# Kernel tuning notes

Measured on AMD Instinct MI355X. Metric: run time of the kernel, lower is better.

## Reference

```python
import jax, jax.numpy as jnp
import numpy as np

FORE_TH = 0.5
BACK_TH = 0.4
MAX_FOR_TARGET = True
FOREGROUND_ONLY = False  # return both foreground and background masks


def _cxcywh_to_xyxy(b):
    cx, cy, w, h = b[..., 0], b[..., 1], b[..., 2], b[..., 3]
    return jnp.stack([cx - w * 0.5, cy - h * 0.5, cx + w * 0.5, cy + h * 0.5], axis=-1)


def _batch_iou(anchors_xyxy, boxes_xyxy):
    # anchors_xyxy: [A,4], boxes_xyxy: [B,T,4] -> ious [B,A,T]
    a = anchors_xyxy[None, :, None, :]   # [1,A,1,4]
    b = boxes_xyxy[:, None, :, :]        # [B,1,T,4]
    lt = jnp.maximum(a[..., :2], b[..., :2])
    rb = jnp.minimum(a[..., 2:], b[..., 2:])
    wh = jnp.clip(rb - lt, 0.0)
    inter = wh[..., 0] * wh[..., 1]                                   # [B,A,T]
    area_a = (a[..., 2] - a[..., 0]) * (a[..., 3] - a[..., 1])
    area_b = (b[..., 2] - b[..., 0]) * (b[..., 3] - b[..., 1])
    return inter / (area_a + area_b - inter + 1e-9)


def setup_inputs() -> dict:
    key = jax.random.key(0)
    k1, k2 = jax.random.split(key)
    labels = jax.random.uniform(k1, (8, 64, 84), dtype=jnp.float32)
    anchors = jax.random.uniform(k2, (1, 100000, 4), dtype=jnp.float32)
    return {"labels": labels, "anchors": anchors}


def reference(labels, anchors):
    # labels: [B, T, 4+C] (cxcywh + class), anchors: [1, A, 4] (cxcywh)
    B = labels.shape[0]
    a_xyxy = _cxcywh_to_xyxy(anchors[0])           # [A,4]
    b_xyxy = _cxcywh_to_xyxy(labels[..., :4])      # [B,T,4]
    ious = _batch_iou(a_xyxy, b_xyxy)              # [B,A,T]

    max_iou_anchor = jnp.max(ious, axis=2)         # [B,A] best IoU per anchor
    target_for_anchor = jnp.argmax(ious, axis=2)   # [B,A] best target per anchor

    fore_mask = max_iou_anchor >= FORE_TH          # [B,A]
    if MAX_FOR_TARGET:
        anchor_for_target = jnp.argmax(ious, axis=1)        # [B,T] best anchor per target
        batch_idx = jnp.arange(B)[:, None]
        fm_t = jnp.zeros(fore_mask.shape, dtype=bool).at[batch_idx, anchor_for_target].set(True)
        fore_mask = jnp.logical_or(fore_mask, fm_t)

    back_mask = jnp.logical_not(fore_mask)
    if BACK_TH is not None:
        back_mask = jnp.logical_and(back_mask, max_iou_anchor < BACK_TH)

    # label[target_for_anchor] per batch -> [B, A, 4+C]
    assigned_target = jnp.take_along_axis(labels, target_for_anchor[..., None], axis=1)

    # Fixed-shape equivalent of the original list-of-dicts with nonzero():
    # (foreground mask, background mask, per-anchor assigned labels).
    return fore_mask, back_mask, assigned_target
```

## Files before the change

### kernel.cpp

```cpp
#include <hip/hip_runtime.h>
#include <stdint.h>

typedef unsigned long long u64;

#define N_ANCH 100000
#define BATCH 8
#define NTGT 64
#define NFEAT 84
#define BLK 256
#define NWAVE (BLK / 64)
#define NBX ((N_ANCH + BLK - 1) / BLK)
#define GCHUNK (NFEAT / 4)

template <bool FULL>
__device__ __forceinline__ void iou_loop(
    const int tid, const int wave, const int n, const bool valid,
    const float4* __restrict__ tbox, const float* __restrict__ sarea,
    u64* __restrict__ board, const float* __restrict__ anchors, u64& bestA)
{
#pragma clang fp contract(off)
    const int nld = FULL ? n : (valid ? n : 0);
    const float4 ab = *(const float4*)(anchors + (size_t)nld * 4);
    const float ax1 = ab.x - ab.z * 0.5f;
    const float ay1 = ab.y - ab.w * 0.5f;
    const float ax2 = ab.x + ab.z * 0.5f;
    const float ay2 = ab.y + ab.w * 0.5f;
    const float areaA = (ax2 - ax1) * (ay2 - ay1);
    const u64 pn = (u64)(0xFFFFFFFFu - (uint32_t)n);

    for (int s = 0; s < NTGT; ++s) {
        const int t = (tid + s) & (NTGT - 1);
        const float4 tb = tbox[t];
        const float areaB = sarea[t];

        const float w = fmaxf(fminf(ax2, tb.z) - fmaxf(ax1, tb.x), 0.0f);
        const float h = fmaxf(fminf(ay2, tb.w) - fmaxf(ay1, tb.y), 0.0f);
        const float inter = w * h;
        const float iou = inter / (((areaA + areaB) - inter) + 1e-9f);
        const uint32_t ib = __float_as_uint(iou);

        const u64 pa = ((u64)ib << 32) | (u64)(63 - t);
        bestA = pa > bestA ? pa : bestA;

        u64 c = ((u64)ib << 32) | pn;
        if (!FULL) c = valid ? c : 0ull;
        atomicMax(&board[(size_t)wave * NTGT + t], c);
    }
}

__global__ __launch_bounds__(BLK) void fused_kernel(
    const float* __restrict__ labels,
    const float* __restrict__ anchors,
    float* __restrict__ out_fore,
    float* __restrict__ out_back,
    float* __restrict__ out_assigned,
    u64* __restrict__ ws_part)
{
#pragma clang fp contract(off)
    __shared__ float4 tbox[NTGT];
    __shared__ float sarea[NTGT];
    __shared__ u64 board[NWAVE * NTGT];
    __shared__ int sidx[BLK];

    const int b    = blockIdx.y;
    const int bx   = blockIdx.x;
    const int tid  = threadIdx.x;
    const int wave = tid >> 6;

    if (tid < NTGT) {
        const float4 box = *(const float4*)(labels + ((size_t)b * NTGT + tid) * NFEAT);
        const float x1 = box.x - box.z * 0.5f;
        const float y1 = box.y - box.w * 0.5f;
        const float x2 = box.x + box.z * 0.5f;
        const float y2 = box.y + box.w * 0.5f;
        tbox[tid] = make_float4(x1, y1, x2, y2);
        sarea[tid] = (x2 - x1) * (y2 - y1);
    }
    board[tid] = 0ull;
    __syncthreads();

    const int n = bx * BLK + tid;
    u64 bestA = 0ull;
    bool valid = true;
    if (bx != NBX - 1) {
        iou_loop<true>(tid, wave, n, true, tbox, sarea, board, anchors, bestA);
    } else {
        valid = (n < N_ANCH);
        iou_loop<false>(tid, wave, n, valid, tbox, sarea, board, anchors, bestA);
    }

    if (valid) {
        const float mi = __uint_as_float((uint32_t)(bestA >> 32));
        const int   bt = 63 - (int)(bestA & 0xFFFFFFFFull);
        const bool fore = (mi >= 0.5f);
        const bool back = (!fore) && (mi < 0.4f);
        const size_t o = (size_t)b * N_ANCH + n;
        out_fore[o] = fore ? 1.0f : 0.0f;
        out_back[o] = back ? 1.0f : 0.0f;
        sidx[tid] = bt;
    } else {
        sidx[tid] = 0;
    }
    __syncthreads();

    if (tid < NTGT) {
        const u64 m0 = board[tid];
        const u64 m1 = board[NTGT + tid];
        const u64 m2 = board[2 * NTGT + tid];
        const u64 m3 = board[3 * NTGT + tid];
        const u64 a = m0 > m1 ? m0 : m1;
        const u64 c = m2 > m3 ? m2 : m3;
        ws_part[((size_t)b * NTGT + tid) * NBX + bx] = a > c ? a : c;
    }

    const float* lab_b = labels + (size_t)b * NTGT * NFEAT;
    float* out_b = out_assigned + ((size_t)b * N_ANCH + (size_t)bx * BLK) * NFEAT;
    for (int i = tid; i < BLK * GCHUNK; i += BLK) {
        const int nl = i / GCHUNK;
        const int k  = i - nl * GCHUNK;
        if (bx * BLK + nl < N_ANCH) {
            const int t = sidx[nl];
            const float4 v = *(const float4*)(lab_b + (size_t)t * NFEAT + k * 4);
            *(float4*)(out_b + (size_t)nl * NFEAT + (size_t)k * 4) = v;
        }
    }
}

__global__ __launch_bounds__(64) void fixup_kernel(
    const u64* __restrict__ ws_part,
    float* __restrict__ out_fore,
    float* __restrict__ out_back)
{
    const int bt   = blockIdx.x;
    const int lane = threadIdx.x;
    const u64* p = ws_part + (size_t)bt * NBX;

    u64 best = 0ull;
    for (int i = lane; i < NBX; i += 64) {
        const u64 v = p[i];
        best = v > best ? v : best;
    }
    for (int off = 32; off > 0; off >>= 1) {
        const u64 o = __shfl_down(best, off, 64);
        best = o > best ? o : best;
    }
    if (lane == 0) {
        const uint32_t n = 0xFFFFFFFFu - (uint32_t)(best & 0xFFFFFFFFull);
        const int b = bt >> 6;
        const size_t o = (size_t)b * N_ANCH + n;
        out_fore[o] = 1.0f;
        out_back[o] = 0.0f;
    }
}

extern "C" void kernel_launch(void* const* d_in, const int* in_sizes, int n_in,
                              void* d_out, int out_size, void* d_ws, size_t ws_size,
                              hipStream_t stream) {
    const float* labels  = (const float*)d_in[0];
    const float* anchors = (const float*)d_in[1];

    float* out_fore     = (float*)d_out;
    float* out_back     = out_fore + (size_t)BATCH * N_ANCH;
    float* out_assigned = out_back + (size_t)BATCH * N_ANCH;

    u64* ws_part = (u64*)d_ws;

    dim3 gridA(NBX, BATCH);
    fused_kernel<<<gridA, BLK, 0, stream>>>(labels, anchors, out_fore, out_back,
                                            out_assigned, ws_part);

    fixup_kernel<<<BATCH * NTGT, 64, 0, stream>>>(ws_part, out_fore, out_back);
}
```

Baseline: 294.7 us.

## Process 1024 anchors per block, pair IoU atomics, overlap gather with compute

Each block now handles 1024 anchors (four per thread) instead of 256. Two anchors share each shared-memory atomicMax on the per-target board, which halves the atomic traffic. The label gather for the first half is interleaved with the IoU loop for the second half, so the stores can overlap compute. Output stores become nontemporal. Fewer blocks means fewer partial results for the fixup pass, at the cost of more registers and less parallelism per block.

```diff
diff --git a/kernel.cpp b/kernel.cpp
--- a/kernel.cpp
+++ b/kernel.cpp
@@ -2,6 +2,7 @@
 #include <stdint.h>
 
 typedef unsigned long long u64;
+typedef __attribute__((__vector_size__(16))) float vfloat4;
 
 #define N_ANCH 100000
 #define BATCH 8
@@ -9,98 +10,149 @@
 #define NFEAT 84
 #define BLK 256
 #define NWAVE (BLK / 64)
-#define NBX ((N_ANCH + BLK - 1) / BLK)
+#define APB 1024
+#define NBX ((N_ANCH + APB - 1) / APB)
 #define GCHUNK (NFEAT / 4)
+#define HALF (APB / 2)
+#define SITER (HALF * GCHUNK / BLK)
+
+struct Anch { float x1, y1, x2, y2, area; u64 pn; };
+
+__device__ __forceinline__ Anch make_anch(float4 ab, int n) {
+#pragma clang fp contract(off)
+    Anch a;
+    a.x1 = ab.x - ab.z * 0.5f;
+    a.y1 = ab.y - ab.w * 0.5f;
+    a.x2 = ab.x + ab.z * 0.5f;
+    a.y2 = ab.y + ab.w * 0.5f;
+    a.area = (a.x2 - a.x1) * (a.y2 - a.y1);
+    a.pn = (u64)(0xFFFFFFFFu - (uint32_t)n);
+    return a;
+}
+
+__device__ __forceinline__ uint32_t iou_bits(const Anch& a, float4 tb, float areaB) {
+#pragma clang fp contract(off)
+    const float w = fmaxf(fminf(a.x2, tb.z) - fmaxf(a.x1, tb.x), 0.0f);
+    const float h = fmaxf(fminf(a.y2, tb.w) - fmaxf(a.y1, tb.y), 0.0f);
+    const float inter = w * h;
+    const float iou = inter / (((a.area + areaB) - inter) + 1e-9f);
+    return __float_as_uint(iou);
+}
 
 template <bool FULL>
-__device__ __forceinline__ void iou_loop(
-    const int tid, const int wave, const int n, const bool valid,
+__device__ __forceinline__ void pair_step(
+    int t, const Anch& A, const Anch& B, bool vA, bool vB,
     const float4* __restrict__ tbox, const float* __restrict__ sarea,
-    u64* __restrict__ board, const float* __restrict__ anchors, u64& bestA)
-{
-#pragma clang fp contract(off)
-    const int nld = FULL ? n : (valid ? n : 0);
-    const float4 ab = *(const float4*)(anchors + (size_t)nld * 4);
-    const float ax1 = ab.x - ab.z * 0.5f;
-    const float ay1 = ab.y - ab.w * 0.5f;
-    const float ax2 = ab.x + ab.z * 0.5f;
-    const float ay2 = ab.y + ab.w * 0.5f;
-    const float areaA = (ax2 - ax1) * (ay2 - ay1);
-    const u64 pn = (u64)(0xFFFFFFFFu - (uint32_t)n);
-
+    u64* __restrict__ slot, u64& bestA, u64& bestB)
+{
+    const float4 tb   = tbox[t];
+    const float areaB = sarea[t];
+    const uint32_t ia = iou_bits(A, tb, areaB);
+    const uint32_t ib = iou_bits(B, tb, areaB);
+    const u64 lowt = (u64)(63 - t);
+    const u64 pa = ((u64)ia << 32) | lowt;
+    const u64 pb = ((u64)ib << 32) | lowt;
+    bestA = pa > bestA ? pa : bestA;
+    bestB = pb > bestB ? pb : bestB;
+    u64 cA = ((u64)ia << 32) | A.pn;
+    u64 cB = ((u64)ib << 32) | B.pn;
+    if (!FULL) { if (!vA) cA = 0ull; if (!vB) cB = 0ull; }
+    const u64 c = cA > cB ? cA : cB;
+    atomicMax(slot + t, c);
+}
+
+__device__ __forceinline__ void write_masks(u64 best, int b, int n,
+                                            float* __restrict__ out_fore,
+                                            float* __restrict__ out_back)
+{
+    const float mi = __uint_as_float((uint32_t)(best >> 32));
+    const bool fore = (mi >= 0.5f);
+    const bool back = (!fore) && (mi < 0.4f);
+    const size_t o = (size_t)b * N_ANCH + n;
+    out_fore[o] = fore ? 1.0f : 0.0f;
+    out_back[o] = back ? 1.0f : 0.0f;
+}
+
+template <bool FULL>
+__device__ __forceinline__ void gather_iter(
+    int j, int tid, int arow0, const int* __restrict__ sidx,
+    const float* __restrict__ lab_b, float* __restrict__ outp)
+{
+    const int i  = j * BLK + tid;
+    const int nl = i / GCHUNK;
+    const int k  = i - nl * GCHUNK;
+    if (FULL || (arow0 + nl < N_ANCH)) {
+        const int t = sidx[nl];
+        const vfloat4 v = *(const vfloat4*)(lab_b + (size_t)t * NFEAT + (size_t)k * 4);
+        __builtin_nontemporal_store(v, (vfloat4*)(outp + (size_t)i * 4));
+    }
+}
+
+template <bool FULL>
+__device__ __forceinline__ void block_body(
+    int b, int bx, int tid, int wave,
+    const float* __restrict__ labels, const float* __restrict__ anchors,
+    float* __restrict__ out_fore, float* __restrict__ out_back,
+    float* __restrict__ out_assigned, u64* __restrict__ ws_part,
+    const float4* __restrict__ tbox, const float* __restrict__ sarea,
+    u64* __restrict__ board, int* __restrict__ sidx)
+{
+    const int base = bx * APB;
+    const int nA0 = base + tid,        nA1 = base + 256 + tid;
+    const int nB0 = base + 512 + tid,  nB1 = base + 768 + tid;
+    const bool vA0 = FULL || (nA0 < N_ANCH);
+    const bool vA1 = FULL || (nA1 < N_ANCH);
+    const bool vB0 = FULL || (nB0 < N_ANCH);
+    const bool vB1 = FULL || (nB1 < N_ANCH);
+
+    const float4 rA0 = *(const float4*)(anchors + (size_t)(vA0 ? nA0 : 0) * 4);
+    const float4 rA1 = *(const float4*)(anchors + (size_t)(vA1 ? nA1 : 0) * 4);
+    const float4 rB0 = *(const float4*)(anchors + (size_t)(vB0 ? nB0 : 0) * 4);
+    const float4 rB1 = *(const float4*)(anchors + (size_t)(vB1 ? nB1 : 0) * 4);
+
+    u64* slot = board + (size_t)wave * NTGT;
+
+    const Anch A0 = make_anch(rA0, nA0), A1 = make_anch(rA1, nA1);
+    u64 bA0 = 0ull, bA1 = 0ull;
+    int t = tid & (NTGT - 1);
+#pragma unroll 4
     for (int s = 0; s < NTGT; ++s) {
-        const int t = (tid + s) & (NTGT - 1);
-        const float4 tb = tbox[t];
-        const float areaB = sarea[t];
-
-        const float w = fmaxf(fminf(ax2, tb.z) - fmaxf(ax1, tb.x), 0.0f);
-        const float h = fmaxf(fminf(ay2, tb.w) - fmaxf(ay1, tb.y), 0.0f);
-        const float inter = w * h;
-        const float iou = inter / (((areaA + areaB) - inter) + 1e-9f);
-        const uint32_t ib = __float_as_uint(iou);
-
-        const u64 pa = ((u64)ib << 32) | (u64)(63 - t);
-        bestA = pa > bestA ? pa : bestA;
-
-        u64 c = ((u64)ib << 32) | pn;
-        if (!FULL) c = valid ? c : 0ull;
-        atomicMax(&board[(size_t)wave * NTGT + t], c);
-    }
-}
-
-__global__ __launch_bounds__(BLK) void fused_kernel(
-    const float* __restrict__ labels,
-    const float* __restrict__ anchors,
-    float* __restrict__ out_fore,
-    float* __restrict__ out_back,
-    float* __restrict__ out_assigned,
-    u64* __restrict__ ws_part)
-{
-#pragma clang fp contract(off)
-    __shared__ float4 tbox[NTGT];
-    __shared__ float sarea[NTGT];
-    __shared__ u64 board[NWAVE * NTGT];
-    __shared__ int sidx[BLK];
-
-    const int b    = blockIdx.y;
-    const int bx   = blockIdx.x;
-    const int tid  = threadIdx.x;
-    const int wave = tid >> 6;
-
-    if (tid < NTGT) {
-        const float4 box = *(const float4*)(labels + ((size_t)b * NTGT + tid) * NFEAT);
-        const float x1 = box.x - box.z * 0.5f;
-        const float y1 = box.y - box.w * 0.5f;
-        const float x2 = box.x + box.z * 0.5f;
-        const float y2 = box.y + box.w * 0.5f;
-        tbox[tid] = make_float4(x1, y1, x2, y2);
-        sarea[tid] = (x2 - x1) * (y2 - y1);
-    }
-    board[tid] = 0ull;
+        pair_step<FULL>(t, A0, A1, vA0, vA1, tbox, sarea, slot, bA0, bA1);
+        t = (t + 1) & (NTGT - 1);
+    }
+
+    if (vA0) { write_masks(bA0, b, nA0, out_fore, out_back);
+               sidx[tid]       = 63 - (int)(bA0 & 0xFFFFFFFFull); }
+    else       sidx[tid]       = 0;
+    if (vA1) { write_masks(bA1, b, nA1, out_fore, out_back);
+               sidx[256 + tid] = 63 - (int)(bA1 & 0xFFFFFFFFull); }
+    else       sidx[256 + tid] = 0;
     __syncthreads();
 
-    const int n = bx * BLK + tid;
-    u64 bestA = 0ull;
-    bool valid = true;
-    if (bx != NBX - 1) {
-        iou_loop<true>(tid, wave, n, true, tbox, sarea, board, anchors, bestA);
-    } else {
-        valid = (n < N_ANCH);
-        iou_loop<false>(tid, wave, n, valid, tbox, sarea, board, anchors, bestA);
-    }
-
-    if (valid) {
-        const float mi = __uint_as_float((uint32_t)(bestA >> 32));
-        const int   bt = 63 - (int)(bestA & 0xFFFFFFFFull);
-        const bool fore = (mi >= 0.5f);
-        const bool back = (!fore) && (mi < 0.4f);
-        const size_t o = (size_t)b * N_ANCH + n;
-        out_fore[o] = fore ? 1.0f : 0.0f;
-        out_back[o] = back ? 1.0f : 0.0f;
-        sidx[tid] = bt;
-    } else {
-        sidx[tid] = 0;
-    }
+    const Anch B0 = make_anch(rB0, nB0), B1 = make_anch(rB1, nB1);
+    u64 bB0 = 0ull, bB1 = 0ull;
+    const float* lab_b = labels + (size_t)b * NTGT * NFEAT;
+    float* out0 = out_assigned + ((size_t)b * N_ANCH + base) * NFEAT;
+
+    t = tid & (NTGT - 1);
+    for (int g = 0; g < 21; ++g) {
+        pair_step<FULL>(t, B0, B1, vB0, vB1, tbox, sarea, slot, bB0, bB1);
+        t = (t + 1) & (NTGT - 1);
+        pair_step<FULL>(t, B0, B1, vB0, vB1, tbox, sarea, slot, bB0, bB1);
+        t = (t + 1) & (NTGT - 1);
+        pair_step<FULL>(t, B0, B1, vB0, vB1, tbox, sarea, slot, bB0, bB1);
+        t = (t + 1) & (NTGT - 1);
+        gather_iter<FULL>(2 * g,     tid, base, sidx, lab_b, out0);
+        gather_iter<FULL>(2 * g + 1, tid, base, sidx, lab_b, out0);
+    }
+    pair_step<FULL>(t, B0, B1, vB0, vB1, tbox, sarea, slot, bB0, bB1);
+
+    if (vB0) { write_masks(bB0, b, nB0, out_fore, out_back);
+               sidx[512 + tid] = 63 - (int)(bB0 & 0xFFFFFFFFull); }
+    else       sidx[512 + tid] = 0;
+    if (vB1) { write_masks(bB1, b, nB1, out_fore, out_back);
+               sidx[768 + tid] = 63 - (int)(bB1 & 0xFFFFFFFFull); }
+    else       sidx[768 + tid] = 0;
     __syncthreads();
 
     if (tid < NTGT) {
@@ -113,16 +165,50 @@
         ws_part[((size_t)b * NTGT + tid) * NBX + bx] = a > c ? a : c;
     }
 
-    const float* lab_b = labels + (size_t)b * NTGT * NFEAT;
-    float* out_b = out_assigned + ((size_t)b * N_ANCH + (size_t)bx * BLK) * NFEAT;
-    for (int i = tid; i < BLK * GCHUNK; i += BLK) {
-        const int nl = i / GCHUNK;
-        const int k  = i - nl * GCHUNK;
-        if (bx * BLK + nl < N_ANCH) {
-            const int t = sidx[nl];
-            const float4 v = *(const float4*)(lab_b + (size_t)t * NFEAT + k * 4);
-            *(float4*)(out_b + (size_t)nl * NFEAT + (size_t)k * 4) = v;
-        }
+    float* out1 = out_assigned + ((size_t)b * N_ANCH + base + HALF) * NFEAT;
+    const int* sidx1 = sidx + HALF;
+#pragma unroll 2
+    for (int j = 0; j < SITER; ++j)
+        gather_iter<FULL>(j, tid, base + HALF, sidx1, lab_b, out1);
+}
+
+__global__ __launch_bounds__(BLK) void fused_kernel(
+    const float* __restrict__ labels,
+    const float* __restrict__ anchors,
+    float* __restrict__ out_fore,
+    float* __restrict__ out_back,
+    float* __restrict__ out_assigned,
+    u64* __restrict__ ws_part)
+{
+#pragma clang fp contract(off)
+    __shared__ float4 tbox[NTGT];
+    __shared__ float  sarea[NTGT];
+    __shared__ u64    board[NWAVE * NTGT];
+    __shared__ int    sidx[APB];
+
+    const int b    = blockIdx.y;
+    const int bx   = blockIdx.x;
+    const int tid  = threadIdx.x;
+    const int wave = tid >> 6;
+
+    if (tid < NTGT) {
+        const float4 box = *(const float4*)(labels + ((size_t)b * NTGT + tid) * NFEAT);
+        const float x1 = box.x - box.z * 0.5f;
+        const float y1 = box.y - box.w * 0.5f;
+        const float x2 = box.x + box.z * 0.5f;
+        const float y2 = box.y + box.w * 0.5f;
+        tbox[tid]  = make_float4(x1, y1, x2, y2);
+        sarea[tid] = (x2 - x1) * (y2 - y1);
+    }
+    board[tid] = 0ull;
+    __syncthreads();
+
+    if (bx != NBX - 1) {
+        block_body<true >(b, bx, tid, wave, labels, anchors, out_fore, out_back,
+                          out_assigned, ws_part, tbox, sarea, board, sidx);
+    } else {
+        block_body<false>(b, bx, tid, wave, labels, anchors, out_fore, out_back,
+                          out_assigned, ws_part, tbox, sarea, board, sidx);
     }
 }
 
```

Result: slower. 307.7 us (+4.4%).
